# Optimization experiments

Hardware: AMD Instinct MI355X
Metric: run time of the kernel (lower is better)

Reference implementation:

```python
import jax, jax.numpy as jnp
import numpy as np

B, N, VD, AD, SD, HD = 32, 2048, 512, 128, 128, 64

def _lin_params(key, out_d, in_d, scale=0.05):
    k1, k2 = jax.random.split(key)
    w = jax.random.normal(k1, (out_d, in_d), jnp.float32) * scale
    b = jax.random.normal(k2, (out_d,), jnp.float32) * scale
    return w, b

def setup_inputs() -> dict:
    key = jax.random.key(0)
    ks = jax.random.split(key, 10)
    inp = {
        'vfeat': jax.random.normal(ks[0], (B, N, VD), jnp.float32),
        'afeat': jax.random.normal(ks[1], (B, N, AD), jnp.float32),
    }
    inp['vfc_w'], inp['vfc_b'] = _lin_params(ks[2], SD, VD)
    inp['afc_w'], inp['afc_b'] = _lin_params(ks[3], SD, AD)
    inp['am_w'],  inp['am_b']  = _lin_params(ks[4], SD, SD)
    inp['U_w'],   inp['U_b']   = _lin_params(ks[5], HD, SD)
    inp['V_w'],   inp['V_b']   = _lin_params(ks[6], HD, SD)
    inp['W_w'],   inp['W_b']   = _lin_params(ks[7], 1, HD)
    inp['cls_w'], inp['cls_b'] = _lin_params(ks[8], 2, SD)
    return inp

def reference(vfeat, afeat, vfc_w, vfc_b, afc_w, afc_b, am_w, am_b,
              U_w, U_b, V_w, V_b, W_w, W_b, cls_w, cls_b):
    # eval mode: dropout = identity, no softmax on scores
    vo1 = jax.nn.relu(jnp.einsum('bnd,kd->bnk', vfeat, vfc_w) + vfc_b)   # [B,N,128]
    ax = jax.nn.relu(jnp.einsum('bnd,kd->bnk', afeat, afc_w) + afc_b)    # [B,N,128]
    # AM (gated cross-modal attention): attfeat = vo1 * sigmoid(Linear(ax))
    gate = jax.nn.sigmoid(jnp.einsum('bnk,jk->bnj', ax, am_w) + am_b)
    ffeat = vo1 * gate + vo1                                             # attfeat + vo1
    # gated attention score head
    v = jax.nn.relu(jnp.einsum('bnk,hk->bnh', ffeat, V_w) + V_b)
    u = jax.nn.sigmoid(jnp.einsum('bnk,hk->bnh', ffeat, U_w) + U_b)
    scores = jnp.einsum('bnh,oh->bno', v * u, W_w) + W_b                 # [B,N,1]
    s = scores[..., 0]                                                   # [B,N]
    # attention-weighted pooling (batched mm replaces per-sample loop)
    zfeat = jnp.einsum('bn,bnk->bk', s, ffeat)                           # [B,128]
    logits = jnp.einsum('bk,ck->bc', zfeat, cls_w) + cls_b               # [B,2]
    return (s, logits)
```

## Files before the change

### kernel.cpp

```cpp
#include <hip/hip_runtime.h>
#include <hip/hip_bf16.h>

#define B_   32
#define N_   2048
#define VD_  512
#define AD_  128
#define SD_  128
#define TM   128
#define THREADS 512

typedef __attribute__((ext_vector_type(8))) short short8;
typedef __attribute__((ext_vector_type(4))) float f32x4;

#define WOFF_VFC 0
#define WOFF_AFC 65536
#define WOFF_AM  81920
#define WOFF_V   98304
#define WOFF_U   106496
#define WTOT     114688

__device__ __forceinline__ float sigmoidf_(float x) { return 1.0f / (1.0f + __expf(-x)); }

__device__ __forceinline__ ushort f2bf(float x) {
    union { float f; unsigned int i; } v; v.f = x;
    unsigned int r = v.i + 0x7FFFu + ((v.i >> 16) & 1u);
    return (ushort)(r >> 16);
}
__device__ __forceinline__ float bf2f(ushort u) {
    union { unsigned int i; float f; } v; v.i = ((unsigned int)u) << 16; return v.f;
}
__device__ __forceinline__ int swz(int row, int k, int ldk) {
    return row * ldk + (k ^ ((row & 7) << 3));
}
__device__ __forceinline__ int fswz(int row, int c) {
    return row * 32 + ((c ^ (row & 7)) << 2);
}
__device__ __forceinline__ short8 pack8(float4 x, float4 y) {
    short8 r;
    r[0] = (short)f2bf(x.x); r[1] = (short)f2bf(x.y); r[2] = (short)f2bf(x.z); r[3] = (short)f2bf(x.w);
    r[4] = (short)f2bf(y.x); r[5] = (short)f2bf(y.y); r[6] = (short)f2bf(y.z); r[7] = (short)f2bf(y.w);
    return r;
}

__device__ __forceinline__ void stage_tile32(const float* __restrict__ src, int ldK, int kcol,
                                             float* lds_base, int wid, int lane)
{
    #pragma unroll
    for (int i = 0; i < 2; ++i) {
        int D   = i * 512 + wid * 64 + lane;
        int row = D >> 3, jj = D & 7;
        int j   = jj ^ (row & 7);
        const float* gp = src + (size_t)row * ldK + kcol + j * 4;
        float* lp = lds_base + (size_t)(i * 512 + wid * 64) * 4;
        __builtin_amdgcn_global_load_lds((const __attribute__((address_space(1))) void*)gp,
                                         (__attribute__((address_space(3))) void*)lp, 16, 0, 0);
    }
}

__global__ __launch_bounds__(256)
void cvt_weights(const float* __restrict__ vfc, const float* __restrict__ afc,
                 const float* __restrict__ am,  const float* __restrict__ Vw,
                 const float* __restrict__ Uw,  ushort* __restrict__ dst)
{
    int f = blockIdx.x * 256 + threadIdx.x;
    if (f >= WTOT / 8) return;
    int e0 = f * 8;
    const float* src; int base, K;
    if      (e0 < WOFF_AFC) { src = vfc; base = WOFF_VFC; K = 512; }
    else if (e0 < WOFF_AM)  { src = afc; base = WOFF_AFC; K = 128; }
    else if (e0 < WOFF_V)   { src = am;  base = WOFF_AM;  K = 128; }
    else if (e0 < WOFF_U)   { src = Vw;  base = WOFF_V;   K = 128; }
    else                    { src = Uw;  base = WOFF_U;   K = 128; }
    int lf = f - base / 8;
    int l = lf & 63, rem = lf >> 6;
    int NK = K / 32;
    int kc = rem % NK, n = rem / NK;
    int tc = l & 15, g4 = l >> 4;
    const float* sp = src + (size_t)(n * 16 + tc) * K + kc * 32 + g4 * 8;
    float4 x = ((const float4*)sp)[0], y = ((const float4*)sp)[1];
    short8 o = pack8(x, y);
    *(short8*)(dst + e0) = o;
}

template<int K>
__device__ __forceinline__ void gemm_staged(const float* __restrict__ Asrc,
                                            const ushort* __restrict__ Bp,
                                            float* Ab0, float* Ab1,
                                            int wid, int lane, int wr, int wc, int t16, int g4,
                                            f32x4 (&acc)[2][4])
{
    constexpr int NC = K / 32;
    const ushort* bp = Bp + (size_t)(4 * wc) * NC * 512 + lane * 8;
    short8 pb[4];
    #pragma unroll
    for (int n = 0; n < 4; ++n) pb[n] = *(const short8*)(bp + (size_t)n * NC * 512);

    #pragma unroll
    for (int kc = 0; kc < NC; ++kc) {
        float* cur = (kc & 1) ? Ab1 : Ab0;
        float* nxt = (kc & 1) ? Ab0 : Ab1;
        __syncthreads();
        if (kc + 1 < NC) stage_tile32(Asrc, K, (kc + 1) * 32, nxt, wid, lane);
        int row0 = 32 * wr + t16, row1 = row0 + 16;
        float4 x0 = *(const float4*)&cur[fswz(row0, 2 * g4)];
        float4 y0 = *(const float4*)&cur[fswz(row0, 2 * g4 + 1)];
        float4 x1 = *(const float4*)&cur[fswz(row1, 2 * g4)];
        float4 y1 = *(const float4*)&cur[fswz(row1, 2 * g4 + 1)];
        short8 a0 = pack8(x0, y0), a1 = pack8(x1, y1);
        short8 b0 = pb[0], b1 = pb[1], b2 = pb[2], b3 = pb[3];
        if (kc + 1 < NC) {
            #pragma unroll
            for (int n = 0; n < 4; ++n)
                pb[n] = *(const short8*)(bp + (size_t)(kc + 1) * 512 + (size_t)n * NC * 512);
        }
        acc[0][0] = __builtin_amdgcn_mfma_f32_16x16x32_bf16(a0, b0, acc[0][0], 0, 0, 0);
        acc[1][0] = __builtin_amdgcn_mfma_f32_16x16x32_bf16(a1, b0, acc[1][0], 0, 0, 0);
        acc[0][1] = __builtin_amdgcn_mfma_f32_16x16x32_bf16(a0, b1, acc[0][1], 0, 0, 0);
        acc[1][1] = __builtin_amdgcn_mfma_f32_16x16x32_bf16(a1, b1, acc[1][1], 0, 0, 0);
        acc[0][2] = __builtin_amdgcn_mfma_f32_16x16x32_bf16(a0, b2, acc[0][2], 0, 0, 0);
        acc[1][2] = __builtin_amdgcn_mfma_f32_16x16x32_bf16(a1, b2, acc[1][2], 0, 0, 0);
        acc[0][3] = __builtin_amdgcn_mfma_f32_16x16x32_bf16(a0, b3, acc[0][3], 0, 0, 0);
        acc[1][3] = __builtin_amdgcn_mfma_f32_16x16x32_bf16(a1, b3, acc[1][3], 0, 0, 0);
    }
}

template<int K>
__device__ __forceinline__ void gemm_lp(const ushort* __restrict__ Ab,
                                        const ushort* __restrict__ Bp,
                                        int wr, int wc, int t16, int g4, int lane,
                                        f32x4 (&acc)[2][4])
{
    constexpr int NK = K / 32;
    const ushort* bp = Bp + (size_t)(4 * wc) * NK * 512 + lane * 8;
    short8 pb[4];
    #pragma unroll
    for (int n = 0; n < 4; ++n) pb[n] = *(const short8*)(bp + (size_t)n * NK * 512);

    #pragma unroll
    for (int kc = 0; kc < NK; ++kc) {
        int k = kc * 32 + g4 * 8;
        short8 a0 = *(const short8*)&Ab[swz(32 * wr + t16,      k, 128)];
        short8 a1 = *(const short8*)&Ab[swz(32 * wr + 16 + t16, k, 128)];
        short8 b0 = pb[0], b1 = pb[1], b2 = pb[2], b3 = pb[3];
        if (kc + 1 < NK) {
            #pragma unroll
            for (int n = 0; n < 4; ++n)
                pb[n] = *(const short8*)(bp + (size_t)(kc + 1) * 512 + (size_t)n * NK * 512);
        }
        acc[0][0] = __builtin_amdgcn_mfma_f32_16x16x32_bf16(a0, b0, acc[0][0], 0, 0, 0);
        acc[1][0] = __builtin_amdgcn_mfma_f32_16x16x32_bf16(a1, b0, acc[1][0], 0, 0, 0);
        acc[0][1] = __builtin_amdgcn_mfma_f32_16x16x32_bf16(a0, b1, acc[0][1], 0, 0, 0);
        acc[1][1] = __builtin_amdgcn_mfma_f32_16x16x32_bf16(a1, b1, acc[1][1], 0, 0, 0);
        acc[0][2] = __builtin_amdgcn_mfma_f32_16x16x32_bf16(a0, b2, acc[0][2], 0, 0, 0);
        acc[1][2] = __builtin_amdgcn_mfma_f32_16x16x32_bf16(a1, b2, acc[1][2], 0, 0, 0);
        acc[0][3] = __builtin_amdgcn_mfma_f32_16x16x32_bf16(a0, b3, acc[0][3], 0, 0, 0);
        acc[1][3] = __builtin_amdgcn_mfma_f32_16x16x32_bf16(a1, b3, acc[1][3], 0, 0, 0);
    }
}

__global__ __launch_bounds__(THREADS, 4)
void fused_mil(const float* __restrict__ vfeat, const float* __restrict__ afeat,
               const ushort* __restrict__ wsW,
               const float* __restrict__ afc_b, const float* __restrict__ am_b,
               const float* __restrict__ vfc_b,
               const float* __restrict__ V_b,   const float* __restrict__ U_b,
               const float* __restrict__ W_w,   const float* __restrict__ W_b,
               float* __restrict__ s_out, float* __restrict__ zpart)
{
    __shared__ __align__(16) ushort Xbuf[128 * 128];
    __shared__ __align__(16) float  Abuf[2][128 * 32];
    __shared__ float sP[2][128];
    __shared__ float sS[128];
    __shared__ float zq[4][128];

    const int tid  = threadIdx.x;
    const int bx   = blockIdx.x;
    const int b    = bx >> 4;
    const int tok0 = (bx & 15) * TM;
    const int wid  = tid >> 6;
    const int lane = tid & 63;
    const int t16  = lane & 15;
    const int g4   = lane >> 4;
    const int wr   = wid >> 1;
    const int wc   = wid & 1;

    const float* afeat_t = afeat + ((size_t)b * N_ + tok0) * AD_;
    const float* vfeat_t = vfeat + ((size_t)b * N_ + tok0) * VD_;

    f32x4 acc[2][4];

    stage_tile32(afeat_t, AD_, 0, Abuf[0], wid, lane);
    #pragma unroll
    for (int m = 0; m < 2; ++m)
        #pragma unroll
        for (int n = 0; n < 4; ++n) acc[m][n] = (f32x4)0.0f;
    gemm_staged<AD_>(afeat_t, wsW + WOFF_AFC, Abuf[0], Abuf[1], wid, lane, wr, wc, t16, g4, acc);
    #pragma unroll
    for (int n = 0; n < 4; ++n) {
        int c = 64 * wc + 16 * n + t16;
        float bias = afc_b[c];
        #pragma unroll
        for (int m = 0; m < 2; ++m)
            #pragma unroll
            for (int r = 0; r < 4; ++r) {
                int row = 32 * wr + 16 * m + 4 * g4 + r;
                Xbuf[swz(row, c, 128)] = f2bf(fmaxf(acc[m][n][r] + bias, 0.0f));
            }
    }
    __syncthreads();

    stage_tile32(vfeat_t, VD_, 0, Abuf[0], wid, lane);

    #pragma unroll
    for (int m = 0; m < 2; ++m)
        #pragma unroll
        for (int n = 0; n < 4; ++n) acc[m][n] = (f32x4)0.0f;
    gemm_lp<SD_>(Xbuf, wsW + WOFF_AM, wr, wc, t16, g4, lane, acc);
    __syncthreads();
    #pragma unroll
    for (int n = 0; n < 4; ++n) {
        int c = 64 * wc + 16 * n + t16;
        float bias = am_b[c];
        #pragma unroll
        for (int m = 0; m < 2; ++m)
            #pragma unroll
            for (int r = 0; r < 4; ++r) {
                int row = 32 * wr + 16 * m + 4 * g4 + r;
                Xbuf[swz(row, c, 128)] = f2bf(sigmoidf_(acc[m][n][r] + bias));
            }
    }

    #pragma unroll
    for (int m = 0; m < 2; ++m)
        #pragma unroll
        for (int n = 0; n < 4; ++n) acc[m][n] = (f32x4)0.0f;
    gemm_staged<VD_>(vfeat_t, wsW + WOFF_VFC, Abuf[0], Abuf[1], wid, lane, wr, wc, t16, g4, acc);

    #pragma unroll
    for (int n = 0; n < 4; ++n) {
        int c = 64 * wc + 16 * n + t16;
        float vb = vfc_b[c];
        #pragma unroll
        for (int m = 0; m < 2; ++m)
            #pragma unroll
            for (int r = 0; r < 4; ++r) {
                int row = 32 * wr + 16 * m + 4 * g4 + r;
                float g   = bf2f(Xbuf[swz(row, c, 128)]);
                float vo1 = fmaxf(acc[m][n][r] + vb, 0.0f);
                Xbuf[swz(row, c, 128)] = f2bf(vo1 * (1.0f + g));
            }
    }
    __syncthreads();

    #pragma unroll
    for (int m = 0; m < 2; ++m)
        #pragma unroll
        for (int n = 0; n < 4; ++n) acc[m][n] = (f32x4)0.0f;
    {
        const ushort* Vp = wsW + WOFF_V;
        const ushort* Up = wsW + WOFF_U;
        short8 pb[4];
        pb[0] = *(const short8*)(Vp + ((size_t)(2 * wc + 0) * 4 + 0) * 512 + lane * 8);
        pb[1] = *(const short8*)(Vp + ((size_t)(2 * wc + 1) * 4 + 0) * 512 + lane * 8);
        pb[2] = *(const short8*)(Up + ((size_t)(2 * wc + 0) * 4 + 0) * 512 + lane * 8);
        pb[3] = *(const short8*)(Up + ((size_t)(2 * wc + 1) * 4 + 0) * 512 + lane * 8);
        #pragma unroll
        for (int kc = 0; kc < 4; ++kc) {
            int k = kc * 32 + g4 * 8;
            short8 a0 = *(const short8*)&Xbuf[swz(32 * wr + t16,      k, 128)];
            short8 a1 = *(const short8*)&Xbuf[swz(32 * wr + 16 + t16, k, 128)];
            short8 b0 = pb[0], b1 = pb[1], b2 = pb[2], b3 = pb[3];
            if (kc < 3) {
                pb[0] = *(const short8*)(Vp + ((size_t)(2 * wc + 0) * 4 + kc + 1) * 512 + lane * 8);
                pb[1] = *(const short8*)(Vp + ((size_t)(2 * wc + 1) * 4 + kc + 1) * 512 + lane * 8);
                pb[2] = *(const short8*)(Up + ((size_t)(2 * wc + 0) * 4 + kc + 1) * 512 + lane * 8);
                pb[3] = *(const short8*)(Up + ((size_t)(2 * wc + 1) * 4 + kc + 1) * 512 + lane * 8);
            }
            acc[0][0] = __builtin_amdgcn_mfma_f32_16x16x32_bf16(a0, b0, acc[0][0], 0, 0, 0);
            acc[1][0] = __builtin_amdgcn_mfma_f32_16x16x32_bf16(a1, b0, acc[1][0], 0, 0, 0);
            acc[0][1] = __builtin_amdgcn_mfma_f32_16x16x32_bf16(a0, b1, acc[0][1], 0, 0, 0);
            acc[1][1] = __builtin_amdgcn_mfma_f32_16x16x32_bf16(a1, b1, acc[1][1], 0, 0, 0);
            acc[0][2] = __builtin_amdgcn_mfma_f32_16x16x32_bf16(a0, b2, acc[0][2], 0, 0, 0);
            acc[1][2] = __builtin_amdgcn_mfma_f32_16x16x32_bf16(a1, b2, acc[1][2], 0, 0, 0);
            acc[0][3] = __builtin_amdgcn_mfma_f32_16x16x32_bf16(a0, b3, acc[0][3], 0, 0, 0);
            acc[1][3] = __builtin_amdgcn_mfma_f32_16x16x32_bf16(a1, b3, acc[1][3], 0, 0, 0);
        }
    }

    #pragma unroll
    for (int m = 0; m < 2; ++m)
        #pragma unroll
        for (int r = 0; r < 4; ++r) {
            float p = 0.0f;
            #pragma unroll
            for (int n = 0; n < 2; ++n) {
                int h = 32 * wc + 16 * n + t16;
                float vv = fmaxf(acc[m][n][r] + V_b[h], 0.0f);
                float uu = sigmoidf_(acc[m][n + 2][r] + U_b[h]);
                p = fmaf(vv * uu, W_w[h], p);
            }
            p += __shfl_xor(p, 1);
            p += __shfl_xor(p, 2);
            p += __shfl_xor(p, 4);
            p += __shfl_xor(p, 8);
            if (t16 == 0) sP[wc][32 * wr + 16 * m + 4 * g4 + r] = p;
        }
    __syncthreads();
    if (tid < 128) {
        float s = sP[0][tid] + sP[1][tid] + W_b[0];
        sS[tid] = s;
        s_out[(size_t)b * N_ + tok0 + tid] = s;
    }
    __syncthreads();

    {
        int k = tid & 127, q = tid >> 7;
        float z = 0.0f;
        #pragma unroll
        for (int t = 0; t < 32; ++t) {
            int row = q * 32 + t;
            z = fmaf(sS[row], bf2f(Xbuf[swz(row, k, 128)]), z);
        }
        zq[q][k] = z;
    }
    __syncthreads();
    if (tid < 128)
        zpart[(size_t)bx * 128 + tid] = zq[0][tid] + zq[1][tid] + zq[2][tid] + zq[3][tid];
}

__global__ __launch_bounds__(128)
void reduce_logits(const float* __restrict__ zpart,
                   const float* __restrict__ cls_w, const float* __restrict__ cls_b,
                   float* __restrict__ out)
{
    __shared__ float sZ[128];
    int b = blockIdx.x, k = threadIdx.x;
    float z = 0.0f;
    #pragma unroll
    for (int t = 0; t < 16; ++t) z += zpart[(size_t)(b * 16 + t) * 128 + k];
    sZ[k] = z;
    __syncthreads();
    if (k < 2) {
        float acc = cls_b[k];
        for (int i = 0; i < 128; ++i) acc = fmaf(sZ[i], cls_w[k * 128 + i], acc);
        out[(size_t)B_ * N_ + b * 2 + k] = acc;
    }
}

extern "C" void kernel_launch(void* const* d_in, const int* in_sizes, int n_in,
                              void* d_out, int out_size, void* d_ws, size_t ws_size,
                              hipStream_t stream) {
    const float* vfeat = (const float*)d_in[0];
    const float* afeat = (const float*)d_in[1];
    const float* vfc_w = (const float*)d_in[2];
    const float* vfc_b = (const float*)d_in[3];
    const float* afc_w = (const float*)d_in[4];
    const float* afc_b = (const float*)d_in[5];
    const float* am_w  = (const float*)d_in[6];
    const float* am_b  = (const float*)d_in[7];
    const float* U_w   = (const float*)d_in[8];
    const float* U_b   = (const float*)d_in[9];
    const float* V_w   = (const float*)d_in[10];
    const float* V_b   = (const float*)d_in[11];
    const float* W_w   = (const float*)d_in[12];
    const float* W_b   = (const float*)d_in[13];
    const float* cls_w = (const float*)d_in[14];
    const float* cls_b = (const float*)d_in[15];

    float* out   = (float*)d_out;
    ushort* wsW  = (ushort*)d_ws;
    float* zpart = (float*)((char*)d_ws + (size_t)WTOT * 2);

    cvt_weights<<<dim3((WTOT / 8 + 255) / 256), dim3(256), 0, stream>>>(vfc_w, afc_w, am_w, V_w, U_w, wsW);
    fused_mil<<<dim3(B_ * 16), dim3(THREADS), 0, stream>>>(
        vfeat, afeat, wsW, afc_b, am_b, vfc_b, V_b, U_b, W_w, W_b, out, zpart);
    reduce_logits<<<dim3(B_), dim3(128), 0, stream>>>(zpart, cls_w, cls_b, out);
}
```

Measured before the change: 52.03 us.

## Halve token tile, triple-buffer staged loads with vmcnt waits, use packed bf16 convert

The token tile per block drops from 128 to 64 and threads from 512 to 256, doubling the grid to 1024 blocks. The staged A-operand pipeline moves from double to triple buffering with a prefetch distance of two. Explicit s_waitcnt vmcnt waits and raw s_barrier replace the __syncthreads calls, and B fragments are double-buffered in registers. The scalar float-to-bf16 rounding is replaced by v_cvt_pk_bf16_f32 inline asm, and scratch arrays are aliased into the A buffer to save LDS. This aims to hide global load latency and raise occupancy, at the cost of more blocks, more partial sums to reduce, and fragile hand-counted wait counts.

Result: slower. 57.15 us (+9.8%).

```diff
diff --git a/kernel.cpp b/kernel.cpp
--- a/kernel.cpp
+++ b/kernel.cpp
@@ -6,8 +6,8 @@
 #define VD_  512
 #define AD_  128
 #define SD_  128
-#define TM   128
-#define THREADS 512
+#define TM   64
+#define THREADS 256
 
 typedef __attribute__((ext_vector_type(8))) short short8;
 typedef __attribute__((ext_vector_type(4))) float f32x4;
@@ -36,22 +36,28 @@
     return row * 32 + ((c ^ (row & 7)) << 2);
 }
 __device__ __forceinline__ short8 pack8(float4 x, float4 y) {
-    short8 r;
-    r[0] = (short)f2bf(x.x); r[1] = (short)f2bf(x.y); r[2] = (short)f2bf(x.z); r[3] = (short)f2bf(x.w);
-    r[4] = (short)f2bf(y.x); r[5] = (short)f2bf(y.y); r[6] = (short)f2bf(y.z); r[7] = (short)f2bf(y.w);
-    return r;
-}
-
-__device__ __forceinline__ void stage_tile32(const float* __restrict__ src, int ldK, int kcol,
-                                             float* lds_base, int wid, int lane)
+    union { unsigned int u[4]; short8 s; } o;
+    asm("v_cvt_pk_bf16_f32 %0, %1, %2" : "=v"(o.u[0]) : "v"(x.x), "v"(x.y));
+    asm("v_cvt_pk_bf16_f32 %0, %1, %2" : "=v"(o.u[1]) : "v"(x.z), "v"(x.w));
+    asm("v_cvt_pk_bf16_f32 %0, %1, %2" : "=v"(o.u[2]) : "v"(y.x), "v"(y.y));
+    asm("v_cvt_pk_bf16_f32 %0, %1, %2" : "=v"(o.u[3]) : "v"(y.z), "v"(y.w));
+    return o.s;
+}
+template<int N> __device__ __forceinline__ void vmwait() {
+    if constexpr (N == 0) asm volatile("s_waitcnt vmcnt(0)" ::: "memory");
+    else if constexpr (N == 6) asm volatile("s_waitcnt vmcnt(6)" ::: "memory");
+}
+
+__device__ __forceinline__ void stage64(const float* __restrict__ src, int ldK, int kcol,
+                                        float* lds_base, int wid, int lane)
 {
     #pragma unroll
     for (int i = 0; i < 2; ++i) {
-        int D   = i * 512 + wid * 64 + lane;
+        int D   = i * 256 + wid * 64 + lane;
         int row = D >> 3, jj = D & 7;
         int j   = jj ^ (row & 7);
         const float* gp = src + (size_t)row * ldK + kcol + j * 4;
-        float* lp = lds_base + (size_t)(i * 512 + wid * 64) * 4;
+        float* lp = lds_base + (i * 256 + wid * 64) * 4;
         __builtin_amdgcn_global_load_lds((const __attribute__((address_space(1))) void*)gp,
                                          (__attribute__((address_space(3))) void*)lp, 16, 0, 0);
     }
@@ -83,36 +89,48 @@
 }
 
 template<int K>
-__device__ __forceinline__ void gemm_staged(const float* __restrict__ Asrc,
-                                            const ushort* __restrict__ Bp,
-                                            float* Ab0, float* Ab1,
-                                            int wid, int lane, int wr, int wc, int t16, int g4,
-                                            f32x4 (&acc)[2][4])
+__device__ __forceinline__ void stage_head(const float* __restrict__ Asrc,
+                                           float (*Ab)[TM * 32], int wid, int lane)
+{
+    stage64(Asrc, K, 0,  Ab[0], wid, lane);
+    stage64(Asrc, K, 32, Ab[1], wid, lane);
+}
+
+template<int K>
+__device__ __forceinline__ void pipe_loop(const float* __restrict__ Asrc,
+                                          const ushort* __restrict__ Bp,
+                                          float (*Ab)[TM * 32],
+                                          int wid, int lane, int wr, int wc, int t16, int g4,
+                                          f32x4 (&acc)[2][4])
 {
     constexpr int NC = K / 32;
     const ushort* bp = Bp + (size_t)(4 * wc) * NC * 512 + lane * 8;
-    short8 pb[4];
-    #pragma unroll
-    for (int n = 0; n < 4; ++n) pb[n] = *(const short8*)(bp + (size_t)n * NC * 512);
+    short8 pbuf[2][4];
+    #pragma unroll
+    for (int n = 0; n < 4; ++n) pbuf[0][n] = *(const short8*)(bp + (size_t)n * NC * 512);
+    #pragma unroll
+    for (int n = 0; n < 4; ++n) pbuf[1][n] = *(const short8*)(bp + 512 + (size_t)n * NC * 512);
 
     #pragma unroll
     for (int kc = 0; kc < NC; ++kc) {
-        float* cur = (kc & 1) ? Ab1 : Ab0;
-        float* nxt = (kc & 1) ? Ab0 : Ab1;
-        __syncthreads();
-        if (kc + 1 < NC) stage_tile32(Asrc, K, (kc + 1) * 32, nxt, wid, lane);
-        int row0 = 32 * wr + t16, row1 = row0 + 16;
-        float4 x0 = *(const float4*)&cur[fswz(row0, 2 * g4)];
-        float4 y0 = *(const float4*)&cur[fswz(row0, 2 * g4 + 1)];
-        float4 x1 = *(const float4*)&cur[fswz(row1, 2 * g4)];
-        float4 y1 = *(const float4*)&cur[fswz(row1, 2 * g4 + 1)];
+        if (kc + 1 < NC) vmwait<6>(); else vmwait<0>();
+        __builtin_amdgcn_s_barrier();
+        __builtin_amdgcn_sched_barrier(0);
+        short8 b0 = pbuf[kc & 1][0], b1 = pbuf[kc & 1][1];
+        short8 b2 = pbuf[kc & 1][2], b3 = pbuf[kc & 1][3];
+        if (kc + 2 < NC) {
+            stage64(Asrc, K, (kc + 2) * 32, Ab[(kc + 2) % 3], wid, lane);
+            #pragma unroll
+            for (int n = 0; n < 4; ++n)
+                pbuf[kc & 1][n] = *(const short8*)(bp + (size_t)(kc + 2) * 512 + (size_t)n * NC * 512);
+        }
+        const float* cur = Ab[kc % 3];
+        int row0 = 32 * wr + t16;
+        float4 x0 = *(const float4*)&cur[fswz(row0,      2 * g4)];
+        float4 y0 = *(const float4*)&cur[fswz(row0,      2 * g4 + 1)];
+        float4 x1 = *(const float4*)&cur[fswz(row0 + 16, 2 * g4)];
+        float4 y1 = *(const float4*)&cur[fswz(row0 + 16, 2 * g4 + 1)];
         short8 a0 = pack8(x0, y0), a1 = pack8(x1, y1);
-        short8 b0 = pb[0], b1 = pb[1], b2 = pb[2], b3 = pb[3];
-        if (kc + 1 < NC) {
-            #pragma unroll
-            for (int n = 0; n < 4; ++n)
-                pb[n] = *(const short8*)(bp + (size_t)(kc + 1) * 512 + (size_t)n * NC * 512);
-        }
         acc[0][0] = __builtin_amdgcn_mfma_f32_16x16x32_bf16(a0, b0, acc[0][0], 0, 0, 0);
         acc[1][0] = __builtin_amdgcn_mfma_f32_16x16x32_bf16(a1, b0, acc[1][0], 0, 0, 0);
         acc[0][1] = __builtin_amdgcn_mfma_f32_16x16x32_bf16(a0, b1, acc[0][1], 0, 0, 0);
@@ -167,16 +185,17 @@
                const float* __restrict__ W_w,   const float* __restrict__ W_b,
                float* __restrict__ s_out, float* __restrict__ zpart)
 {
-    __shared__ __align__(16) ushort Xbuf[128 * 128];
-    __shared__ __align__(16) float  Abuf[2][128 * 32];
-    __shared__ float sP[2][128];
-    __shared__ float sS[128];
-    __shared__ float zq[4][128];
+    __shared__ __align__(16) ushort Xbuf[TM * 128];
+    __shared__ __align__(16) float  Abuf[3][TM * 32];
+
+    float* sPb = (float*)Abuf;
+    float* sSb = sPb + 128;
+    float* zqb = sSb + 64;
 
     const int tid  = threadIdx.x;
     const int bx   = blockIdx.x;
-    const int b    = bx >> 4;
-    const int tok0 = (bx & 15) * TM;
+    const int b    = bx >> 5;
+    const int tok0 = (bx & 31) * TM;
     const int wid  = tid >> 6;
     const int lane = tid & 63;
     const int t16  = lane & 15;
@@ -189,12 +208,12 @@
 
     f32x4 acc[2][4];
 
-    stage_tile32(afeat_t, AD_, 0, Abuf[0], wid, lane);
+    stage_head<AD_>(afeat_t, Abuf, wid, lane);
     #pragma unroll
     for (int m = 0; m < 2; ++m)
         #pragma unroll
         for (int n = 0; n < 4; ++n) acc[m][n] = (f32x4)0.0f;
-    gemm_staged<AD_>(afeat_t, wsW + WOFF_AFC, Abuf[0], Abuf[1], wid, lane, wr, wc, t16, g4, acc);
+    pipe_loop<AD_>(afeat_t, wsW + WOFF_AFC, Abuf, wid, lane, wr, wc, t16, g4, acc);
     #pragma unroll
     for (int n = 0; n < 4; ++n) {
         int c = 64 * wc + 16 * n + t16;
@@ -209,7 +228,7 @@
     }
     __syncthreads();
 
-    stage_tile32(vfeat_t, VD_, 0, Abuf[0], wid, lane);
+    stage_head<VD_>(vfeat_t, Abuf, wid, lane);
 
     #pragma unroll
     for (int m = 0; m < 2; ++m)
@@ -234,7 +253,7 @@
     for (int m = 0; m < 2; ++m)
         #pragma unroll
         for (int n = 0; n < 4; ++n) acc[m][n] = (f32x4)0.0f;
-    gemm_staged<VD_>(vfeat_t, wsW + WOFF_VFC, Abuf[0], Abuf[1], wid, lane, wr, wc, t16, g4, acc);
+    pipe_loop<VD_>(vfeat_t, wsW + WOFF_VFC, Abuf, wid, lane, wr, wc, t16, g4, acc);
 
     #pragma unroll
     for (int n = 0; n < 4; ++n) {
@@ -303,12 +322,12 @@
             p += __shfl_xor(p, 2);
             p += __shfl_xor(p, 4);
             p += __shfl_xor(p, 8);
-            if (t16 == 0) sP[wc][32 * wr + 16 * m + 4 * g4 + r] = p;
-        }
-    __syncthreads();
-    if (tid < 128) {
-        float s = sP[0][tid] + sP[1][tid] + W_b[0];
-        sS[tid] = s;
+            if (t16 == 0) sPb[wc * 64 + 32 * wr + 16 * m + 4 * g4 + r] = p;
+        }
+    __syncthreads();
+    if (tid < TM) {
+        float s = sPb[tid] + sPb[64 + tid] + W_b[0];
+        sSb[tid] = s;
         s_out[(size_t)b * N_ + tok0 + tid] = s;
     }
     __syncthreads();
@@ -319,13 +338,13 @@
         #pragma unroll
         for (int t = 0; t < 32; ++t) {
             int row = q * 32 + t;
-            z = fmaf(sS[row], bf2f(Xbuf[swz(row, k, 128)]), z);
-        }
-        zq[q][k] = z;
+            z = fmaf(sSb[row], bf2f(Xbuf[swz(row, k, 128)]), z);
+        }
+        zqb[q * 128 + k] = z;
     }
     __syncthreads();
     if (tid < 128)
-        zpart[(size_t)bx * 128 + tid] = zq[0][tid] + zq[1][tid] + zq[2][tid] + zq[3][tid];
+        zpart[(size_t)bx * 128 + tid] = zqb[tid] + zqb[128 + tid];
 }
 
 __global__ __launch_bounds__(128)
@@ -337,7 +356,7 @@
     int b = blockIdx.x, k = threadIdx.x;
     float z = 0.0f;
     #pragma unroll
-    for (int t = 0; t < 16; ++t) z += zpart[(size_t)(b * 16 + t) * 128 + k];
+    for (int t = 0; t < 32; ++t) z += zpart[(size_t)(b * 32 + t) * 128 + k];
     sZ[k] = z;
     __syncthreads();
     if (k < 2) {
@@ -372,7 +391,7 @@
     float* zpart = (float*)((char*)d_ws + (size_t)WTOT * 2);
 
     cvt_weights<<<dim3((WTOT / 8 + 255) / 256), dim3(256), 0, stream>>>(vfc_w, afc_w, am_w, V_w, U_w, wsW);
-    fused_mil<<<dim3(B_ * 16), dim3(THREADS), 0, stream>>>(
+    fused_mil<<<dim3(B_ * 32), dim3(THREADS), 0, stream>>>(
         vfeat, afeat, wsW, afc_b, am_b, vfc_b, V_b, U_b, W_w, W_b, out, zpart);
     reduce_logits<<<dim3(B_), dim3(128), 0, stream>>>(zpart, cls_w, cls_b, out);
 }
```

## Merge vfc and afc GEMMs into one 5-stage async LDS pipeline with staged weights

Applied to the files above, without the earlier changes.

Replaces the two separate double-buffered GEMM loops with a single 20-chunk loop covering the vfeat (512-wide) and afeat (128-wide) projections. It uses a 5-slot ring with 4 chunks in flight, and both activations and packed bf16 weights are loaded with global_load_lds, synchronised by explicit vmcnt waits and raw barriers. It also switches fp32-to-bf16 packing to the hardware v_cvt_pk_bf16_f32 instruction and reuses the ring buffers for the reduction scratch. The aim is to hide global memory latency with deeper prefetch. The cost is much more shared memory: launch bounds drop to 1 block per SM and occupancy falls.

After: 59.70 us. 1.15x slower.

```diff
diff --git a/kernel.cpp b/kernel.cpp
--- a/kernel.cpp
+++ b/kernel.cpp
@@ -36,25 +36,23 @@
     return row * 32 + ((c ^ (row & 7)) << 2);
 }
 __device__ __forceinline__ short8 pack8(float4 x, float4 y) {
-    short8 r;
-    r[0] = (short)f2bf(x.x); r[1] = (short)f2bf(x.y); r[2] = (short)f2bf(x.z); r[3] = (short)f2bf(x.w);
-    r[4] = (short)f2bf(y.x); r[5] = (short)f2bf(y.y); r[6] = (short)f2bf(y.z); r[7] = (short)f2bf(y.w);
-    return r;
-}
-
-__device__ __forceinline__ void stage_tile32(const float* __restrict__ src, int ldK, int kcol,
-                                             float* lds_base, int wid, int lane)
-{
-    #pragma unroll
-    for (int i = 0; i < 2; ++i) {
-        int D   = i * 512 + wid * 64 + lane;
-        int row = D >> 3, jj = D & 7;
-        int j   = jj ^ (row & 7);
-        const float* gp = src + (size_t)row * ldK + kcol + j * 4;
-        float* lp = lds_base + (size_t)(i * 512 + wid * 64) * 4;
-        __builtin_amdgcn_global_load_lds((const __attribute__((address_space(1))) void*)gp,
-                                         (__attribute__((address_space(3))) void*)lp, 16, 0, 0);
-    }
+    union { unsigned int u[4]; short8 s; } o;
+    asm("v_cvt_pk_bf16_f32 %0, %1, %2" : "=v"(o.u[0]) : "v"(x.x), "v"(x.y));
+    asm("v_cvt_pk_bf16_f32 %0, %1, %2" : "=v"(o.u[1]) : "v"(x.z), "v"(x.w));
+    asm("v_cvt_pk_bf16_f32 %0, %1, %2" : "=v"(o.u[2]) : "v"(y.x), "v"(y.y));
+    asm("v_cvt_pk_bf16_f32 %0, %1, %2" : "=v"(o.u[3]) : "v"(y.z), "v"(y.w));
+    return o.s;
+}
+template<int N> __device__ __forceinline__ void vm_wait() {
+    if constexpr (N == 0) asm volatile("s_waitcnt vmcnt(0)" ::: "memory");
+    else if constexpr (N == 3) asm volatile("s_waitcnt vmcnt(3)" ::: "memory");
+    else if constexpr (N == 6) asm volatile("s_waitcnt vmcnt(6)" ::: "memory");
+    else asm volatile("s_waitcnt vmcnt(9)" ::: "memory");
+}
+__device__ __forceinline__ void lds_sync() {
+    asm volatile("s_waitcnt lgkmcnt(0)" ::: "memory");
+    __builtin_amdgcn_s_barrier();
+    __builtin_amdgcn_sched_barrier(0);
 }
 
 __global__ __launch_bounds__(256)
@@ -82,83 +80,46 @@
     *(short8*)(dst + e0) = o;
 }
 
-template<int K>
-__device__ __forceinline__ void gemm_staged(const float* __restrict__ Asrc,
-                                            const ushort* __restrict__ Bp,
-                                            float* Ab0, float* Ab1,
-                                            int wid, int lane, int wr, int wc, int t16, int g4,
-                                            f32x4 (&acc)[2][4])
-{
-    constexpr int NC = K / 32;
-    const ushort* bp = Bp + (size_t)(4 * wc) * NC * 512 + lane * 8;
-    short8 pb[4];
-    #pragma unroll
-    for (int n = 0; n < 4; ++n) pb[n] = *(const short8*)(bp + (size_t)n * NC * 512);
-
-    #pragma unroll
-    for (int kc = 0; kc < NC; ++kc) {
-        float* cur = (kc & 1) ? Ab1 : Ab0;
-        float* nxt = (kc & 1) ? Ab0 : Ab1;
-        __syncthreads();
-        if (kc + 1 < NC) stage_tile32(Asrc, K, (kc + 1) * 32, nxt, wid, lane);
-        int row0 = 32 * wr + t16, row1 = row0 + 16;
-        float4 x0 = *(const float4*)&cur[fswz(row0, 2 * g4)];
-        float4 y0 = *(const float4*)&cur[fswz(row0, 2 * g4 + 1)];
-        float4 x1 = *(const float4*)&cur[fswz(row1, 2 * g4)];
-        float4 y1 = *(const float4*)&cur[fswz(row1, 2 * g4 + 1)];
-        short8 a0 = pack8(x0, y0), a1 = pack8(x1, y1);
-        short8 b0 = pb[0], b1 = pb[1], b2 = pb[2], b3 = pb[3];
-        if (kc + 1 < NC) {
-            #pragma unroll
-            for (int n = 0; n < 4; ++n)
-                pb[n] = *(const short8*)(bp + (size_t)(kc + 1) * 512 + (size_t)n * NC * 512);
-        }
-        acc[0][0] = __builtin_amdgcn_mfma_f32_16x16x32_bf16(a0, b0, acc[0][0], 0, 0, 0);
-        acc[1][0] = __builtin_amdgcn_mfma_f32_16x16x32_bf16(a1, b0, acc[1][0], 0, 0, 0);
-        acc[0][1] = __builtin_amdgcn_mfma_f32_16x16x32_bf16(a0, b1, acc[0][1], 0, 0, 0);
-        acc[1][1] = __builtin_amdgcn_mfma_f32_16x16x32_bf16(a1, b1, acc[1][1], 0, 0, 0);
-        acc[0][2] = __builtin_amdgcn_mfma_f32_16x16x32_bf16(a0, b2, acc[0][2], 0, 0, 0);
-        acc[1][2] = __builtin_amdgcn_mfma_f32_16x16x32_bf16(a1, b2, acc[1][2], 0, 0, 0);
-        acc[0][3] = __builtin_amdgcn_mfma_f32_16x16x32_bf16(a0, b3, acc[0][3], 0, 0, 0);
-        acc[1][3] = __builtin_amdgcn_mfma_f32_16x16x32_bf16(a1, b3, acc[1][3], 0, 0, 0);
-    }
-}
-
-template<int K>
-__device__ __forceinline__ void gemm_lp(const ushort* __restrict__ Ab,
-                                        const ushort* __restrict__ Bp,
-                                        int wr, int wc, int t16, int g4, int lane,
-                                        f32x4 (&acc)[2][4])
-{
-    constexpr int NK = K / 32;
-    const ushort* bp = Bp + (size_t)(4 * wc) * NK * 512 + lane * 8;
-    short8 pb[4];
-    #pragma unroll
-    for (int n = 0; n < 4; ++n) pb[n] = *(const short8*)(bp + (size_t)n * NK * 512);
-
-    #pragma unroll
-    for (int kc = 0; kc < NK; ++kc) {
-        int k = kc * 32 + g4 * 8;
-        short8 a0 = *(const short8*)&Ab[swz(32 * wr + t16,      k, 128)];
-        short8 a1 = *(const short8*)&Ab[swz(32 * wr + 16 + t16, k, 128)];
-        short8 b0 = pb[0], b1 = pb[1], b2 = pb[2], b3 = pb[3];
-        if (kc + 1 < NK) {
-            #pragma unroll
-            for (int n = 0; n < 4; ++n)
-                pb[n] = *(const short8*)(bp + (size_t)(kc + 1) * 512 + (size_t)n * NK * 512);
-        }
-        acc[0][0] = __builtin_amdgcn_mfma_f32_16x16x32_bf16(a0, b0, acc[0][0], 0, 0, 0);
-        acc[1][0] = __builtin_amdgcn_mfma_f32_16x16x32_bf16(a1, b0, acc[1][0], 0, 0, 0);
-        acc[0][1] = __builtin_amdgcn_mfma_f32_16x16x32_bf16(a0, b1, acc[0][1], 0, 0, 0);
-        acc[1][1] = __builtin_amdgcn_mfma_f32_16x16x32_bf16(a1, b1, acc[1][1], 0, 0, 0);
-        acc[0][2] = __builtin_amdgcn_mfma_f32_16x16x32_bf16(a0, b2, acc[0][2], 0, 0, 0);
-        acc[1][2] = __builtin_amdgcn_mfma_f32_16x16x32_bf16(a1, b2, acc[1][2], 0, 0, 0);
-        acc[0][3] = __builtin_amdgcn_mfma_f32_16x16x32_bf16(a0, b3, acc[0][3], 0, 0, 0);
-        acc[1][3] = __builtin_amdgcn_mfma_f32_16x16x32_bf16(a1, b3, acc[1][3], 0, 0, 0);
-    }
-}
-
-__global__ __launch_bounds__(THREADS, 4)
+__device__ __forceinline__ void stage_bundle(const float* __restrict__ srcA, int ldK, int kcol,
+                                             const ushort* __restrict__ srcB,
+                                             float* Ab, ushort* Bb, int wid, int lane)
+{
+    #pragma unroll
+    for (int i = 0; i < 2; ++i) {
+        int D   = i * 512 + wid * 64 + lane;
+        int row = D >> 3, jj = D & 7;
+        int j   = jj ^ (row & 7);
+        const float* gp = srcA + (size_t)row * ldK + kcol + j * 4;
+        float* lp = Ab + (i * 512 + wid * 64) * 4;
+        __builtin_amdgcn_global_load_lds((const __attribute__((address_space(1))) void*)gp,
+                                         (__attribute__((address_space(3))) void*)lp, 16, 0, 0);
+    }
+    const ushort* gpb = srcB + lane * 8;
+    ushort* lpb = Bb + wid * 512;
+    __builtin_amdgcn_global_load_lds((const __attribute__((address_space(1))) void*)gpb,
+                                     (__attribute__((address_space(3))) void*)lpb, 16, 0, 0);
+}
+
+__device__ __forceinline__ void chunk_mfma(const float* __restrict__ Ab,
+                                           const ushort* __restrict__ Bb,
+                                           int wr, int wc, int t16, int g4, int lane,
+                                           f32x4 (&acc)[2][4])
+{
+    int row0 = 32 * wr + t16;
+    float4 x0 = *(const float4*)&Ab[fswz(row0,      2 * g4)];
+    float4 y0 = *(const float4*)&Ab[fswz(row0,      2 * g4 + 1)];
+    float4 x1 = *(const float4*)&Ab[fswz(row0 + 16, 2 * g4)];
+    float4 y1 = *(const float4*)&Ab[fswz(row0 + 16, 2 * g4 + 1)];
+    short8 a0 = pack8(x0, y0), a1 = pack8(x1, y1);
+    #pragma unroll
+    for (int n = 0; n < 4; ++n) {
+        short8 b = *(const short8*)&Bb[(4 * wc + n) * 512 + lane * 8];
+        acc[0][n] = __builtin_amdgcn_mfma_f32_16x16x32_bf16(a0, b, acc[0][n], 0, 0, 0);
+        acc[1][n] = __builtin_amdgcn_mfma_f32_16x16x32_bf16(a1, b, acc[1][n], 0, 0, 0);
+    }
+}
+
+__global__ __launch_bounds__(THREADS, 1)
 void fused_mil(const float* __restrict__ vfeat, const float* __restrict__ afeat,
                const ushort* __restrict__ wsW,
                const float* __restrict__ afc_b, const float* __restrict__ am_b,
@@ -167,11 +128,13 @@
                const float* __restrict__ W_w,   const float* __restrict__ W_b,
                float* __restrict__ s_out, float* __restrict__ zpart)
 {
+    __shared__ __align__(16) float  Abuf[5][128 * 32];
+    __shared__ __align__(16) ushort Bbuf[5][8 * 512];
     __shared__ __align__(16) ushort Xbuf[128 * 128];
-    __shared__ __align__(16) float  Abuf[2][128 * 32];
-    __shared__ float sP[2][128];
-    __shared__ float sS[128];
-    __shared__ float zq[4][128];
+
+    float* sPb = (float*)&Abuf[0][0];
+    float* sSb = sPb + 256;
+    float* zqb = sSb + 128;
 
     const int tid  = threadIdx.x;
     const int bx   = blockIdx.x;
@@ -187,14 +150,39 @@
     const float* afeat_t = afeat + ((size_t)b * N_ + tok0) * AD_;
     const float* vfeat_t = vfeat + ((size_t)b * N_ + tok0) * VD_;
 
-    f32x4 acc[2][4];
-
-    stage_tile32(afeat_t, AD_, 0, Abuf[0], wid, lane);
+    f32x4 accC[2][4], accA[2][4];
     #pragma unroll
     for (int m = 0; m < 2; ++m)
         #pragma unroll
-        for (int n = 0; n < 4; ++n) acc[m][n] = (f32x4)0.0f;
-    gemm_staged<AD_>(afeat_t, wsW + WOFF_AFC, Abuf[0], Abuf[1], wid, lane, wr, wc, t16, g4, acc);
+        for (int n = 0; n < 4; ++n) { accC[m][n] = (f32x4)0.0f; accA[m][n] = (f32x4)0.0f; }
+
+    #define ISSUE(t)                                                                        \
+        do {                                                                                \
+            if ((t) < 16) stage_bundle(vfeat_t, VD_, (t) * 32,                              \
+                                       wsW + WOFF_VFC + ((size_t)(wid * 16 + (t))) * 512,   \
+                                       Abuf[(t) % 5], Bbuf[(t) % 5], wid, lane);            \
+            else          stage_bundle(afeat_t, AD_, ((t) - 16) * 32,                       \
+                                       wsW + WOFF_AFC + ((size_t)(wid * 4 + (t) - 16)) * 512,\
+                                       Abuf[(t) % 5], Bbuf[(t) % 5], wid, lane);            \
+        } while (0)
+
+    #pragma unroll
+    for (int t = 0; t < 4; ++t) ISSUE(t);
+
+    #pragma unroll
+    for (int k = 0; k < 20; ++k) {
+        if (k < 17)      vm_wait<9>();
+        else if (k == 17) vm_wait<6>();
+        else if (k == 18) vm_wait<3>();
+        else              vm_wait<0>();
+        __builtin_amdgcn_s_barrier();
+        __builtin_amdgcn_sched_barrier(0);
+        if (k + 4 < 20) ISSUE(k + 4);
+        if (k < 16) chunk_mfma(Abuf[k % 5], Bbuf[k % 5], wr, wc, t16, g4, lane, accC);
+        else        chunk_mfma(Abuf[k % 5], Bbuf[k % 5], wr, wc, t16, g4, lane, accA);
+    }
+    #undef ISSUE
+
     #pragma unroll
     for (int n = 0; n < 4; ++n) {
         int c = 64 * wc + 16 * n + t16;
@@ -204,19 +192,30 @@
             #pragma unroll
             for (int r = 0; r < 4; ++r) {
                 int row = 32 * wr + 16 * m + 4 * g4 + r;
-                Xbuf[swz(row, c, 128)] = f2bf(fmaxf(acc[m][n][r] + bias, 0.0f));
-            }
-    }
-    __syncthreads();
-
-    stage_tile32(vfeat_t, VD_, 0, Abuf[0], wid, lane);
-
+                Xbuf[swz(row, c, 128)] = f2bf(fmaxf(accA[m][n][r] + bias, 0.0f));
+            }
+    }
+    lds_sync();
+
+    f32x4 accB[2][4];
     #pragma unroll
     for (int m = 0; m < 2; ++m)
         #pragma unroll
-        for (int n = 0; n < 4; ++n) acc[m][n] = (f32x4)0.0f;
-    gemm_lp<SD_>(Xbuf, wsW + WOFF_AM, wr, wc, t16, g4, lane, acc);
-    __syncthreads();
+        for (int n = 0; n < 4; ++n) accB[m][n] = (f32x4)0.0f;
+    #pragma unroll
+    for (int kc = 0; kc < 4; ++kc) {
+        int kk = kc * 32 + g4 * 8;
+        short8 a0 = *(const short8*)&Xbuf[swz(32 * wr + t16,      kk, 128)];
+        short8 a1 = *(const short8*)&Xbuf[swz(32 * wr + 16 + t16, kk, 128)];
+        #pragma unroll
+        for (int n = 0; n < 4; ++n) {
+            short8 bmat = *(const short8*)(wsW + WOFF_AM + ((size_t)((4 * wc + n) * 4 + kc)) * 512 + lane * 8);
+            accB[0][n] = __builtin_amdgcn_mfma_f32_16x16x32_bf16(a0, bmat, accB[0][n], 0, 0, 0);
+            accB[1][n] = __builtin_amdgcn_mfma_f32_16x16x32_bf16(a1, bmat, accB[1][n], 0, 0, 0);
+        }
+    }
+    lds_sync();
+
     #pragma unroll
     for (int n = 0; n < 4; ++n) {
         int c = 64 * wc + 16 * n + t16;
@@ -226,15 +225,9 @@
             #pragma unroll
             for (int r = 0; r < 4; ++r) {
                 int row = 32 * wr + 16 * m + 4 * g4 + r;
-                Xbuf[swz(row, c, 128)] = f2bf(sigmoidf_(acc[m][n][r] + bias));
-            }
-    }
-
-    #pragma unroll
-    for (int m = 0; m < 2; ++m)
-        #pragma unroll
-        for (int n = 0; n < 4; ++n) acc[m][n] = (f32x4)0.0f;
-    gemm_staged<VD_>(vfeat_t, wsW + WOFF_VFC, Abuf[0], Abuf[1], wid, lane, wr, wc, t16, g4, acc);
+                Xbuf[swz(row, c, 128)] = f2bf(sigmoidf_(accB[m][n][r] + bias));
+            }
+    }
 
     #pragma unroll
     for (int n = 0; n < 4; ++n) {
@@ -246,44 +239,33 @@
             for (int r = 0; r < 4; ++r) {
                 int row = 32 * wr + 16 * m + 4 * g4 + r;
                 float g   = bf2f(Xbuf[swz(row, c, 128)]);
-                float vo1 = fmaxf(acc[m][n][r] + vb, 0.0f);
+                float vo1 = fmaxf(accC[m][n][r] + vb, 0.0f);
                 Xbuf[swz(row, c, 128)] = f2bf(vo1 * (1.0f + g));
             }
     }
-    __syncthreads();
+    lds_sync();
 
     #pragma unroll
     for (int m = 0; m < 2; ++m)
         #pragma unroll
-        for (int n = 0; n < 4; ++n) acc[m][n] = (f32x4)0.0f;
+        for (int n = 0; n < 4; ++n) accB[m][n] = (f32x4)0.0f;
     {
         const ushort* Vp = wsW + WOFF_V;
         const ushort* Up = wsW + WOFF_U;
-        short8 pb[4];
-        pb[0] = *(const short8*)(Vp + ((size_t)(2 * wc + 0) * 4 + 0) * 512 + lane * 8);
-        pb[1] = *(const short8*)(Vp + ((size_t)(2 * wc + 1) * 4 + 0) * 512 + lane * 8);
-        pb[2] = *(const short8*)(Up + ((size_t)(2 * wc + 0) * 4 + 0) * 512 + lane * 8);
-        pb[3] = *(const short8*)(Up + ((size_t)(2 * wc + 1) * 4 + 0) * 512 + lane * 8);
         #pragma unroll
         for (int kc = 0; kc < 4; ++kc) {
-            int k = kc * 32 + g4 * 8;
-            short8 a0 = *(const short8*)&Xbuf[swz(32 * wr + t16,      k, 128)];
-            short8 a1 = *(const short8*)&Xbuf[swz(32 * wr + 16 + t16, k, 128)];
-            short8 b0 = pb[0], b1 = pb[1], b2 = pb[2], b3 = pb[3];
-            if (kc < 3) {
-                pb[0] = *(const short8*)(Vp + ((size_t)(2 * wc + 0) * 4 + kc + 1) * 512 + lane * 8);
-                pb[1] = *(const short8*)(Vp + ((size_t)(2 * wc + 1) * 4 + kc + 1) * 512 + lane * 8);
-                pb[2] = *(const short8*)(Up + ((size_t)(2 * wc + 0) * 4 + kc + 1) * 512 + lane * 8);
-                pb[3] = *(const short8*)(Up + ((size_t)(2 * wc + 1) * 4 + kc + 1) * 512 + lane * 8);
-            }
-            acc[0][0] = __builtin_amdgcn_mfma_f32_16x16x32_bf16(a0, b0, acc[0][0], 0, 0, 0);
-            acc[1][0] = __builtin_amdgcn_mfma_f32_16x16x32_bf16(a1, b0, acc[1][0], 0, 0, 0);
-            acc[0][1] = __builtin_amdgcn_mfma_f32_16x16x32_bf16(a0, b1, acc[0][1], 0, 0, 0);
-            acc[1][1] = __builtin_amdgcn_mfma_f32_16x16x32_bf16(a1, b1, acc[1][1], 0, 0, 0);
-            acc[0][2] = __builtin_amdgcn_mfma_f32_16x16x32_bf16(a0, b2, acc[0][2], 0, 0, 0);
-            acc[1][2] = __builtin_amdgcn_mfma_f32_16x16x32_bf16(a1, b2, acc[1][2], 0, 0, 0);
-            acc[0][3] = __builtin_amdgcn_mfma_f32_16x16x32_bf16(a0, b3, acc[0][3], 0, 0, 0);
-            acc[1][3] = __builtin_amdgcn_mfma_f32_16x16x32_bf16(a1, b3, acc[1][3], 0, 0, 0);
+            int kk = kc * 32 + g4 * 8;
+            short8 a0 = *(const short8*)&Xbuf[swz(32 * wr + t16,      kk, 128)];
+            short8 a1 = *(const short8*)&Xbuf[swz(32 * wr + 16 + t16, kk, 128)];
+            #pragma unroll
+            for (int n = 0; n < 2; ++n) {
+                short8 bv = *(const short8*)(Vp + ((size_t)(2 * wc + n) * 4 + kc) * 512 + lane * 8);
+                short8 bu = *(const short8*)(Up + ((size_t)(2 * wc + n) * 4 + kc) * 512 + lane * 8);
+                accB[0][n]     = __builtin_amdgcn_mfma_f32_16x16x32_bf16(a0, bv, accB[0][n],     0, 0, 0);
+                accB[1][n]     = __builtin_amdgcn_mfma_f32_16x16x32_bf16(a1, bv, accB[1][n],     0, 0, 0);
+                accB[0][n + 2] = __builtin_amdgcn_mfma_f32_16x16x32_bf16(a0, bu, accB[0][n + 2], 0, 0, 0);
+                accB[1][n + 2] = __builtin_amdgcn_mfma_f32_16x16x32_bf16(a1, bu, accB[1][n + 2], 0, 0, 0);
+            }
         }
     }
 
@@ -295,20 +277,20 @@
             #pragma unroll
             for (int n = 0; n < 2; ++n) {
                 int h = 32 * wc + 16 * n + t16;
-                float vv = fmaxf(acc[m][n][r] + V_b[h], 0.0f);
-                float uu = sigmoidf_(acc[m][n + 2][r] + U_b[h]);
+                float vv = fmaxf(accB[m][n][r] + V_b[h], 0.0f);
+                float uu = sigmoidf_(accB[m][n + 2][r] + U_b[h]);
                 p = fmaf(vv * uu, W_w[h], p);
             }
             p += __shfl_xor(p, 1);
             p += __shfl_xor(p, 2);
             p += __shfl_xor(p, 4);
             p += __shfl_xor(p, 8);
-            if (t16 == 0) sP[wc][32 * wr + 16 * m + 4 * g4 + r] = p;
+            if (t16 == 0) sPb[wc * 128 + 32 * wr + 16 * m + 4 * g4 + r] = p;
         }
     __syncthreads();
     if (tid < 128) {
-        float s = sP[0][tid] + sP[1][tid] + W_b[0];
-        sS[tid] = s;
+        float s = sPb[tid] + sPb[128 + tid] + W_b[0];
+        sSb[tid] = s;
         s_out[(size_t)b * N_ + tok0 + tid] = s;
     }
     __syncthreads();
@@ -319,13 +301,13 @@
         #pragma unroll
         for (int t = 0; t < 32; ++t) {
             int row = q * 32 + t;
-            z = fmaf(sS[row], bf2f(Xbuf[swz(row, k, 128)]), z);
+            z = fmaf(sSb[row], bf2f(Xbuf[swz(row, k, 128)]), z);
         }
-        zq[q][k] = z;
+        zqb[q * 128 + k] = z;
     }
     __syncthreads();
     if (tid < 128)
-        zpart[(size_t)bx * 128 + tid] = zq[0][tid] + zq[1][tid] + zq[2][tid] + zq[3][tid];
+        zpart[(size_t)bx * 128 + tid] = zqb[tid] + zqb[128 + tid] + zqb[256 + tid] + zqb[384 + tid];
 }
 
 __global__ __launch_bounds__(128)
```
